# Kernel tuning notes

Hardware: AMD Instinct MI355X
Metric: run time of the kernel (lower is better)

## Reference

```python
import jax, jax.numpy as jnp
import numpy as np

C = 256
NUM_HEADS = 8
HEAD_DIM = C // NUM_HEADS
EPS = 1e-5


def setup_inputs() -> dict:
    key = jax.random.key(0)
    ks = jax.random.split(key, 12)
    b, h, w = 8, 64, 64
    s = 1.0 / np.sqrt(C)
    return {
        "cortical": jax.random.normal(ks[0], (b, C, h, w), jnp.float32),
        "subcortical": jax.random.normal(ks[1], (b, C, h, w), jnp.float32),
        "ventricular": jax.random.normal(ks[2], (b, C, h, w), jnp.float32),
        "in_proj_w": jax.random.uniform(ks[3], (3 * C, C), jnp.float32, -s, s),
        "in_proj_b": jnp.zeros((3 * C,), jnp.float32),
        "out_proj_w": jax.random.uniform(ks[4], (C, C), jnp.float32, -s, s),
        "out_proj_b": jnp.zeros((C,), jnp.float32),
        "ln_gamma": jnp.ones((C,), jnp.float32),
        "ln_beta": jnp.zeros((C,), jnp.float32),
        "conv_w": jax.random.uniform(ks[5], (C, 3 * C), jnp.float32, -1.0 / np.sqrt(3 * C), 1.0 / np.sqrt(3 * C)),
        "conv_b": jnp.zeros((C,), jnp.float32),
    }


def _forward(cortical, subcortical, ventricular,
             in_proj_w, in_proj_b, out_proj_w, out_proj_b,
             ln_gamma, ln_beta, conv_w, conv_b):
    b, c, h, w = cortical.shape
    # stack regions -> tokens of seq_len 3: (b,h,w,3,c) -> (N,3,c)
    regions = jnp.stack([cortical, subcortical, ventricular], axis=1)  # (b,3,c,h,w)
    x = regions.transpose(0, 3, 4, 1, 2).reshape(b * h * w, 3, c)
    # fused QKV projection
    qkv = x @ in_proj_w.T + in_proj_b  # (N,3,3c)
    q, k, v = jnp.split(qkv, 3, axis=-1)
    # split heads: (N,3,H,D)
    def heads(t):
        return t.reshape(-1, 3, NUM_HEADS, HEAD_DIM)
    q, k, v = heads(q), heads(k), heads(v)
    scores = jnp.einsum("nshd,nthd->nhst", q, k) / np.sqrt(HEAD_DIM)
    attn = jax.nn.softmax(scores, axis=-1)
    o = jnp.einsum("nhst,nthd->nshd", attn, v).reshape(-1, 3, c)
    o = o @ out_proj_w.T + out_proj_b
    # residual + LayerNorm over channels
    y = o + x
    mu = y.mean(-1, keepdims=True)
    var = y.var(-1, keepdims=True)
    y = (y - mu) * jax.lax.rsqrt(var + EPS) * ln_gamma + ln_beta
    # (N,3,c) -> (b,h,w,3c) region-major == torch cat along channel dim
    fused = y.reshape(b, h, w, 3 * c)
    out = fused @ conv_w.T + conv_b  # 1x1 conv as matmul
    return out.transpose(0, 3, 1, 2)  # (b,c,h,w)


def reference(cortical, subcortical, ventricular, in_proj_w, in_proj_b,
              out_proj_w, out_proj_b, ln_gamma, ln_beta, conv_w, conv_b):
    return _forward(cortical, subcortical, ventricular, in_proj_w, in_proj_b,
                    out_proj_w, out_proj_b, ln_gamma, ln_beta, conv_w, conv_b)
```

## Files before the change

### kernel.cpp

```cpp
#include <hip/hip_runtime.h>

typedef __bf16 bf16x8 __attribute__((ext_vector_type(8)));
typedef float  f32x4  __attribute__((ext_vector_type(4)));

#define XOFF 0
#define OOFF 49152
#define OBUFSZ 7680
#define PSOFF 64512
#define PQOFF 66048
#define MUOFF 67584
#define RSOFF 67968
#define SMEM_BYTES 68352

static __device__ __forceinline__ unsigned short f2b(float f) {
  __bf16 h = (__bf16)f;
  return __builtin_bit_cast(unsigned short, h);
}

__global__ void convert_weights(const float* __restrict__ w_in,
                                const float* __restrict__ w_out,
                                const float* __restrict__ w_conv,
                                __bf16* __restrict__ ws) {
  int gid = blockIdx.x * 256 + threadIdx.x;
  int i4 = gid * 4;
  const float* src;
  int off;
  if (i4 < 196608)      { src = w_in;   off = i4; }
  else if (i4 < 262144) { src = w_out;  off = i4 - 196608; }
  else                  { src = w_conv; off = i4 - 262144; }
  float4 f = *(const float4*)(src + off);
  ws[i4 + 0] = (__bf16)f.x;
  ws[i4 + 1] = (__bf16)f.y;
  ws[i4 + 2] = (__bf16)f.z;
  ws[i4 + 3] = (__bf16)f.w;
}

__global__ __launch_bounds__(256, 2) void crf_fused(
    const float* __restrict__ cort,
    const float* __restrict__ subc,
    const float* __restrict__ vent,
    const __bf16* __restrict__ w_in,
    const float* __restrict__ b_in,
    const __bf16* __restrict__ w_out,
    const float* __restrict__ b_out,
    const float* __restrict__ gamma,
    const float* __restrict__ beta,
    const __bf16* __restrict__ w_conv,
    const float* __restrict__ b_conv,
    float* __restrict__ out) {
  extern __shared__ char smem[];
  const int tid  = threadIdx.x;
  const int lane = tid & 63;
  const int wv   = tid >> 6;
  const int l15  = lane & 15;
  const int l4   = lane >> 4;
  const int blk  = blockIdx.x;
  const int img  = blk >> 7;
  const int pixbase = (blk & 127) << 5;
  const size_t base = (size_t)img * (256 * 4096) + pixbase;

  {
    const float* rp0 = cort + base;
    const float* rp1 = subc + base;
    const float* rp2 = vent + base;
#pragma unroll
    for (int si = 0; si < 3; ++si) {
      const float* rp = (si == 0) ? rp0 : (si == 1) ? rp1 : rp2;
#pragma unroll
      for (int t = 0; t < 16; ++t) {
        int idx = t * 256 + tid;
        int p   = idx & 31;
        int c   = (idx >> 5) * 2;
        float f0 = rp[(size_t)c * 4096 + p];
        float f1 = rp[(size_t)(c + 1) * 4096 + p];
        int m = si * 32 + p;
        unsigned off = ((unsigned)(m * 512 + c * 2)) ^ ((unsigned)(m & 7) << 4);
        unsigned pack = (unsigned)f2b(f0) | ((unsigned)f2b(f1) << 16);
        *(unsigned*)(smem + XOFF + off) = pack;
      }
    }
  }

  f32x4 accY[6][4] = {};

  __syncthreads();

  const int ph = wv & 1;
  const int hg = wv >> 1;
  const float SC = 0.17677669529663687f;

  for (int hh = 0; hh < 4; ++hh) {
    const int h = hg * 4 + hh;
    f32x4 acc[3][6] = {};
#pragma unroll
    for (int ks = 0; ks < 8; ++ks) {
      const int k0 = ks * 32;
      bf16x8 af[3], bfr[6];
#pragma unroll
      for (int s = 0; s < 3; ++s) {
        int m = s * 32 + ph * 16 + l15;
        unsigned off = ((unsigned)(m * 512 + (k0 + l4 * 8) * 2)) ^ ((unsigned)(m & 7) << 4);
        af[s] = *(const bf16x8*)(smem + XOFF + off);
      }
#pragma unroll
      for (int j = 0; j < 6; ++j) {
        int jb = (j >> 1) * 256 + h * 32 + (j & 1) * 16 + l15;
        bfr[j] = *(const bf16x8*)(w_in + (size_t)jb * 256 + k0 + l4 * 8);
      }
#pragma unroll
      for (int s = 0; s < 3; ++s)
#pragma unroll
        for (int j = 0; j < 6; ++j)
          acc[s][j] = __builtin_amdgcn_mfma_f32_16x16x32_bf16(af[s], bfr[j], acc[s][j], 0, 0, 0);
    }
#pragma unroll
    for (int jq = 0; jq < 2; ++jq) {
      float bq = b_in[h * 32 + jq * 16 + l15];
      float bk = b_in[256 + h * 32 + jq * 16 + l15];
      float bv = b_in[512 + h * 32 + jq * 16 + l15];
#pragma unroll
      for (int s = 0; s < 3; ++s)
#pragma unroll
        for (int r = 0; r < 4; ++r) {
          acc[s][jq][r]     += bq;
          acc[s][2 + jq][r] += bk;
          acc[s][4 + jq][r] += bv;
        }
    }
    char* ob = smem + OOFF + hg * OBUFSZ;
#pragma unroll
    for (int si = 0; si < 3; ++si) {
      float pp[3][4];
#pragma unroll
      for (int ti = 0; ti < 3; ++ti)
#pragma unroll
        for (int r = 0; r < 4; ++r)
          pp[ti][r] = acc[si][0][r] * acc[ti][2][r] + acc[si][1][r] * acc[ti][3][r];
#pragma unroll
      for (int mask = 1; mask <= 8; mask <<= 1)
#pragma unroll
        for (int ti = 0; ti < 3; ++ti)
#pragma unroll
          for (int r = 0; r < 4; ++r)
            pp[ti][r] += __shfl_xor(pp[ti][r], mask);
#pragma unroll
      for (int r = 0; r < 4; ++r) {
        float s0 = pp[0][r] * SC, s1 = pp[1][r] * SC, s2 = pp[2][r] * SC;
        float mx = fmaxf(fmaxf(s0, s1), s2);
        float e0 = __expf(s0 - mx), e1 = __expf(s1 - mx), e2 = __expf(s2 - mx);
        float inv = 1.f / (e0 + e1 + e2);
        e0 *= inv; e1 *= inv; e2 *= inv;
        int m = si * 32 + ph * 16 + l4 * 4 + r;
#pragma unroll
        for (int jq = 0; jq < 2; ++jq) {
          float ov = e0 * acc[0][4 + jq][r] + e1 * acc[1][4 + jq][r] + e2 * acc[2][4 + jq][r];
          *(__bf16*)(ob + m * 80 + (jq * 16 + l15) * 2) = (__bf16)ov;
        }
      }
    }
    __syncthreads();

#pragma unroll
    for (int g = 0; g < 2; ++g) {
      const char* obr = smem + OOFF + g * OBUFSZ;
      const int hB = g * 4 + hh;
      bf16x8 af2[6], bf2[4];
#pragma unroll
      for (int i = 0; i < 6; ++i)
        af2[i] = *(const bf16x8*)(obr + (i * 16 + l15) * 80 + l4 * 16);
#pragma unroll
      for (int j = 0; j < 4; ++j) {
        int jr = wv * 64 + j * 16 + l15;
        bf2[j] = *(const bf16x8*)(w_out + (size_t)jr * 256 + hB * 32 + l4 * 8);
      }
#pragma unroll
      for (int i = 0; i < 6; ++i)
#pragma unroll
        for (int j = 0; j < 4; ++j)
          accY[i][j] = __builtin_amdgcn_mfma_f32_16x16x32_bf16(af2[i], bf2[j], accY[i][j], 0, 0, 0);
    }
    __syncthreads();
  }

  float bo[4], gg[4], bb[4];
#pragma unroll
  for (int j = 0; j < 4; ++j) {
    int jc = wv * 64 + j * 16 + l15;
    bo[j] = b_out[jc];
    gg[j] = gamma[jc];
    bb[j] = beta[jc];
  }
#pragma unroll
  for (int i = 0; i < 6; ++i)
#pragma unroll
    for (int r = 0; r < 4; ++r) {
      int m = i * 16 + l4 * 4 + r;
      float s1 = 0.f, s2 = 0.f;
#pragma unroll
      for (int j = 0; j < 4; ++j) {
        int jc = wv * 64 + j * 16 + l15;
        unsigned xo = ((unsigned)(m * 512 + jc * 2)) ^ ((unsigned)(m & 7) << 4);
        float xv = (float)(*(const __bf16*)(smem + XOFF + xo));
        float v = accY[i][j][r] + bo[j] + xv;
        accY[i][j][r] = v;
        s1 += v;
        s2 += v * v;
      }
      s1 += __shfl_xor(s1, 1); s2 += __shfl_xor(s2, 1);
      s1 += __shfl_xor(s1, 2); s2 += __shfl_xor(s2, 2);
      s1 += __shfl_xor(s1, 4); s2 += __shfl_xor(s2, 4);
      s1 += __shfl_xor(s1, 8); s2 += __shfl_xor(s2, 8);
      if (l15 == 0) {
        *(float*)(smem + PSOFF + (m * 4 + wv) * 4) = s1;
        *(float*)(smem + PQOFF + (m * 4 + wv) * 4) = s2;
      }
    }
  __syncthreads();
  if (tid < 96) {
    float s = 0.f, q = 0.f;
#pragma unroll
    for (int j = 0; j < 4; ++j) {
      s += *(const float*)(smem + PSOFF + (tid * 4 + j) * 4);
      q += *(const float*)(smem + PQOFF + (tid * 4 + j) * 4);
    }
    float mu  = s * (1.f / 256.f);
    float var = q * (1.f / 256.f) - mu * mu;
    *(float*)(smem + MUOFF + tid * 4) = mu;
    *(float*)(smem + RSOFF + tid * 4) = rsqrtf(var + 1e-5f);
  }
  __syncthreads();
#pragma unroll
  for (int i = 0; i < 6; ++i)
#pragma unroll
    for (int r = 0; r < 4; ++r) {
      int m = i * 16 + l4 * 4 + r;
      float mu = *(const float*)(smem + MUOFF + m * 4);
      float rs = *(const float*)(smem + RSOFF + m * 4);
      int s = m >> 5, p = m & 31;
#pragma unroll
      for (int j = 0; j < 4; ++j) {
        int jc = wv * 64 + j * 16 + l15;
        float yv = (accY[i][j][r] - mu) * rs * gg[j] + bb[j];
        int kk = s * 256 + jc;
        unsigned off = ((unsigned)(p * 1536 + kk * 2)) ^ ((unsigned)(p & 7) << 4);
        *(__bf16*)(smem + XOFF + off) = (__bf16)yv;
      }
    }
  __syncthreads();

  {
    f32x4 accC[4][2] = {};
#pragma unroll 4
    for (int ks = 0; ks < 24; ++ks) {
      const int k0 = ks * 32;
      bf16x8 af[4], bfr2[2];
#pragma unroll
      for (int i = 0; i < 4; ++i) {
        int co = wv * 64 + i * 16 + l15;
        af[i] = *(const bf16x8*)(w_conv + (size_t)co * 768 + k0 + l4 * 8);
      }
#pragma unroll
      for (int j = 0; j < 2; ++j) {
        int p = j * 16 + l15;
        unsigned off = ((unsigned)(p * 1536 + (k0 + l4 * 8) * 2)) ^ ((unsigned)(p & 7) << 4);
        bfr2[j] = *(const bf16x8*)(smem + XOFF + off);
      }
#pragma unroll
      for (int i = 0; i < 4; ++i)
#pragma unroll
        for (int j = 0; j < 2; ++j)
          accC[i][j] = __builtin_amdgcn_mfma_f32_16x16x32_bf16(af[i], bfr2[j], accC[i][j], 0, 0, 0);
    }
#pragma unroll
    for (int i = 0; i < 4; ++i)
#pragma unroll
      for (int r = 0; r < 4; ++r) {
        int co = wv * 64 + i * 16 + l4 * 4 + r;
        float cb = b_conv[co];
#pragma unroll
        for (int j = 0; j < 2; ++j)
          out[((size_t)img * 256 + co) * 4096 + pixbase + j * 16 + l15] = accC[i][j][r] + cb;
      }
  }
}

extern "C" void kernel_launch(void* const* d_in, const int* in_sizes, int n_in,
                              void* d_out, int out_size, void* d_ws, size_t ws_size,
                              hipStream_t stream) {
  (void)in_sizes; (void)n_in; (void)out_size; (void)ws_size;
  const float* cort    = (const float*)d_in[0];
  const float* subc    = (const float*)d_in[1];
  const float* vent    = (const float*)d_in[2];
  const float* w_in_f  = (const float*)d_in[3];
  const float* b_in    = (const float*)d_in[4];
  const float* w_out_f = (const float*)d_in[5];
  const float* b_out   = (const float*)d_in[6];
  const float* gamma   = (const float*)d_in[7];
  const float* beta    = (const float*)d_in[8];
  const float* w_conv_f= (const float*)d_in[9];
  const float* b_conv  = (const float*)d_in[10];

  __bf16* ws = (__bf16*)d_ws;
  convert_weights<<<448, 256, 0, stream>>>(w_in_f, w_out_f, w_conv_f, ws);
  crf_fused<<<1024, 256, SMEM_BYTES, stream>>>(
      cort, subc, vent,
      ws,            b_in,
      ws + 196608,   b_out,
      gamma,         beta,
      ws + 262144,   b_conv,
      (float*)d_out);
}
```

Measured before the change: 204.4 us.

## Double-buffer attention output, prefetch QKV weights, vectorize input loads

The attention-output buffer is double-buffered per head iteration, which drops the second barrier per head loop, and its layout switches from padded rows to an XOR swizzle. QKV weight fragments are software-prefetched one k-step ahead into a register double buffer. The input-staging loop now reads float4 along pixels instead of scalar pairs. The bias adds are hoisted to the start of the head loop. The costs are more LDS (larger SMEM_BYTES), higher register pressure from the prefetch buffers, and scalar bf16 LDS stores during staging.

```diff
diff --git a/kernel.cpp b/kernel.cpp
--- a/kernel.cpp
+++ b/kernel.cpp
@@ -5,17 +5,13 @@
 
 #define XOFF 0
 #define OOFF 49152
-#define OBUFSZ 7680
-#define PSOFF 64512
-#define PQOFF 66048
-#define MUOFF 67584
-#define RSOFF 67968
-#define SMEM_BYTES 68352
-
-static __device__ __forceinline__ unsigned short f2b(float f) {
-  __bf16 h = (__bf16)f;
-  return __builtin_bit_cast(unsigned short, h);
-}
+#define OBSZ 6144
+#define PSOFF 73728
+#define PQOFF 75264
+#define MUOFF 76800
+#define RSOFF 77184
+#define SMEM_BYTES 77568
+#define OB(g,b) (smem + OOFF + ((g) * 2 + (b)) * OBSZ)
 
 __global__ void convert_weights(const float* __restrict__ w_in,
                                 const float* __restrict__ w_out,
@@ -67,16 +63,18 @@
     for (int si = 0; si < 3; ++si) {
       const float* rp = (si == 0) ? rp0 : (si == 1) ? rp1 : rp2;
 #pragma unroll
-      for (int t = 0; t < 16; ++t) {
+      for (int t = 0; t < 8; ++t) {
         int idx = t * 256 + tid;
-        int p   = idx & 31;
-        int c   = (idx >> 5) * 2;
-        float f0 = rp[(size_t)c * 4096 + p];
-        float f1 = rp[(size_t)(c + 1) * 4096 + p];
-        int m = si * 32 + p;
-        unsigned off = ((unsigned)(m * 512 + c * 2)) ^ ((unsigned)(m & 7) << 4);
-        unsigned pack = (unsigned)f2b(f0) | ((unsigned)f2b(f1) << 16);
-        *(unsigned*)(smem + XOFF + off) = pack;
+        int p4  = (idx & 7) * 4;
+        int c   = idx >> 3;
+        float4 f = *(const float4*)(rp + (size_t)c * 4096 + p4);
+#pragma unroll
+        for (int k = 0; k < 4; ++k) {
+          int m = si * 32 + p4 + k;
+          unsigned off = ((unsigned)(m * 512 + c * 2)) ^ ((unsigned)(m & 7) << 4);
+          float fv = (k == 0) ? f.x : (k == 1) ? f.y : (k == 2) ? f.z : f.w;
+          *(__bf16*)(smem + XOFF + off) = (__bf16)fv;
+        }
       }
     }
   }
@@ -91,11 +89,28 @@
 
   for (int hh = 0; hh < 4; ++hh) {
     const int h = hg * 4 + hh;
+    float bq0 = b_in[h * 32 + l15],       bq1 = b_in[h * 32 + 16 + l15];
+    float bk0 = b_in[256 + h * 32 + l15], bk1 = b_in[256 + h * 32 + 16 + l15];
+    float bv0 = b_in[512 + h * 32 + l15], bv1 = b_in[512 + h * 32 + 16 + l15];
+
     f32x4 acc[3][6] = {};
+    bf16x8 bb[2][6];
+#pragma unroll
+    for (int j = 0; j < 6; ++j) {
+      int jb = (j >> 1) * 256 + h * 32 + (j & 1) * 16 + l15;
+      bb[0][j] = *(const bf16x8*)(w_in + (size_t)jb * 256 + l4 * 8);
+    }
 #pragma unroll
     for (int ks = 0; ks < 8; ++ks) {
       const int k0 = ks * 32;
-      bf16x8 af[3], bfr[6];
+      if (ks < 7) {
+#pragma unroll
+        for (int j = 0; j < 6; ++j) {
+          int jb = (j >> 1) * 256 + h * 32 + (j & 1) * 16 + l15;
+          bb[(ks + 1) & 1][j] = *(const bf16x8*)(w_in + (size_t)jb * 256 + k0 + 32 + l4 * 8);
+        }
+      }
+      bf16x8 af[3];
 #pragma unroll
       for (int s = 0; s < 3; ++s) {
         int m = s * 32 + ph * 16 + l15;
@@ -103,31 +118,21 @@
         af[s] = *(const bf16x8*)(smem + XOFF + off);
       }
 #pragma unroll
-      for (int j = 0; j < 6; ++j) {
-        int jb = (j >> 1) * 256 + h * 32 + (j & 1) * 16 + l15;
-        bfr[j] = *(const bf16x8*)(w_in + (size_t)jb * 256 + k0 + l4 * 8);
-      }
-#pragma unroll
       for (int s = 0; s < 3; ++s)
 #pragma unroll
         for (int j = 0; j < 6; ++j)
-          acc[s][j] = __builtin_amdgcn_mfma_f32_16x16x32_bf16(af[s], bfr[j], acc[s][j], 0, 0, 0);
-    }
-#pragma unroll
-    for (int jq = 0; jq < 2; ++jq) {
-      float bq = b_in[h * 32 + jq * 16 + l15];
-      float bk = b_in[256 + h * 32 + jq * 16 + l15];
-      float bv = b_in[512 + h * 32 + jq * 16 + l15];
-#pragma unroll
-      for (int s = 0; s < 3; ++s)
-#pragma unroll
-        for (int r = 0; r < 4; ++r) {
-          acc[s][jq][r]     += bq;
-          acc[s][2 + jq][r] += bk;
-          acc[s][4 + jq][r] += bv;
-        }
-    }
-    char* ob = smem + OOFF + hg * OBUFSZ;
+          acc[s][j] = __builtin_amdgcn_mfma_f32_16x16x32_bf16(af[s], bb[ks & 1][j], acc[s][j], 0, 0, 0);
+    }
+#pragma unroll
+    for (int s = 0; s < 3; ++s)
+#pragma unroll
+      for (int r = 0; r < 4; ++r) {
+        acc[s][0][r] += bq0; acc[s][1][r] += bq1;
+        acc[s][2][r] += bk0; acc[s][3][r] += bk1;
+        acc[s][4][r] += bv0; acc[s][5][r] += bv1;
+      }
+
+    char* ob = OB(hg, hh & 1);
 #pragma unroll
     for (int si = 0; si < 3; ++si) {
       float pp[3][4];
@@ -154,41 +159,46 @@
 #pragma unroll
         for (int jq = 0; jq < 2; ++jq) {
           float ov = e0 * acc[0][4 + jq][r] + e1 * acc[1][4 + jq][r] + e2 * acc[2][4 + jq][r];
-          *(__bf16*)(ob + m * 80 + (jq * 16 + l15) * 2) = (__bf16)ov;
+          unsigned off = ((unsigned)(m * 64 + (jq * 16 + l15) * 2)) ^ ((unsigned)(m & 7) << 4);
+          *(__bf16*)(ob + off) = (__bf16)ov;
         }
       }
     }
     __syncthreads();
 
-#pragma unroll
-    for (int g = 0; g < 2; ++g) {
-      const char* obr = smem + OOFF + g * OBUFSZ;
-      const int hB = g * 4 + hh;
-      bf16x8 af2[6], bf2[4];
-#pragma unroll
-      for (int i = 0; i < 6; ++i)
-        af2[i] = *(const bf16x8*)(obr + (i * 16 + l15) * 80 + l4 * 16);
+    {
+      const int b = hh & 1;
+      bf16x8 afA[6], afB[6], bfA[4], bfB[4];
+#pragma unroll
+      for (int i = 0; i < 6; ++i) {
+        int row = i * 16 + l15;
+        unsigned off = ((unsigned)(row * 64 + l4 * 16)) ^ ((unsigned)(row & 7) << 4);
+        afA[i] = *(const bf16x8*)(OB(0, b) + off);
+        afB[i] = *(const bf16x8*)(OB(1, b) + off);
+      }
 #pragma unroll
       for (int j = 0; j < 4; ++j) {
         int jr = wv * 64 + j * 16 + l15;
-        bf2[j] = *(const bf16x8*)(w_out + (size_t)jr * 256 + hB * 32 + l4 * 8);
+        bfA[j] = *(const bf16x8*)(w_out + (size_t)jr * 256 + hh * 32 + l4 * 8);
+        bfB[j] = *(const bf16x8*)(w_out + (size_t)jr * 256 + (4 + hh) * 32 + l4 * 8);
       }
 #pragma unroll
       for (int i = 0; i < 6; ++i)
 #pragma unroll
-        for (int j = 0; j < 4; ++j)
-          accY[i][j] = __builtin_amdgcn_mfma_f32_16x16x32_bf16(af2[i], bf2[j], accY[i][j], 0, 0, 0);
-    }
-    __syncthreads();
-  }
-
-  float bo[4], gg[4], bb[4];
+        for (int j = 0; j < 4; ++j) {
+          accY[i][j] = __builtin_amdgcn_mfma_f32_16x16x32_bf16(afA[i], bfA[j], accY[i][j], 0, 0, 0);
+          accY[i][j] = __builtin_amdgcn_mfma_f32_16x16x32_bf16(afB[i], bfB[j], accY[i][j], 0, 0, 0);
+        }
+    }
+  }
+
+  float bo[4], gg[4], bb2[4];
 #pragma unroll
   for (int j = 0; j < 4; ++j) {
     int jc = wv * 64 + j * 16 + l15;
     bo[j] = b_out[jc];
     gg[j] = gamma[jc];
-    bb[j] = beta[jc];
+    bb2[j] = beta[jc];
   }
 #pragma unroll
   for (int i = 0; i < 6; ++i)
@@ -240,7 +250,7 @@
 #pragma unroll
       for (int j = 0; j < 4; ++j) {
         int jc = wv * 64 + j * 16 + l15;
-        float yv = (accY[i][j][r] - mu) * rs * gg[j] + bb[j];
+        float yv = (accY[i][j][r] - mu) * rs * gg[j] + bb2[j];
         int kk = s * 256 + jc;
         unsigned off = ((unsigned)(p * 1536 + kk * 2)) ^ ((unsigned)(p & 7) << 4);
         *(__bf16*)(smem + XOFF + off) = (__bf16)yv;
```

Result: slower. 240.1 us (+17.4%).

## Widen fused block to 1024 threads with one head per wave pair

Applied to the files above, without the earlier changes.

Each block now launches 16 waves instead of 4, so every head of the QKV and attention stage is handled at once by its own pair of waves instead of looping over heads. The per-head attention outputs are written into one full swizzled LDS tile, and out_proj is done as a single K=256 GEMM with each wave owning 16 output channels. The input load switches to float4 vector reads. This removes the per-head barrier loop and lowers register pressure per wave, but raises LDS use to about 109 KB per block, which limits residency to one block per CU.

```diff
diff --git a/kernel.cpp b/kernel.cpp
--- a/kernel.cpp
+++ b/kernel.cpp
@@ -5,12 +5,11 @@
 
 #define XOFF 0
 #define OOFF 49152
-#define OBUFSZ 7680
-#define PSOFF 64512
-#define PQOFF 66048
-#define MUOFF 67584
-#define RSOFF 67968
-#define SMEM_BYTES 68352
+#define PSOFF 98304
+#define PQOFF 104448
+#define MUOFF 110592
+#define RSOFF 110976
+#define SMEM_BYTES 111360
 
 static __device__ __forceinline__ unsigned short f2b(float f) {
   __bf16 h = (__bf16)f;
@@ -35,7 +34,7 @@
   ws[i4 + 3] = (__bf16)f.w;
 }
 
-__global__ __launch_bounds__(256, 2) void crf_fused(
+__global__ __launch_bounds__(1024) void crf_fused(
     const float* __restrict__ cort,
     const float* __restrict__ subc,
     const float* __restrict__ vent,
@@ -60,42 +59,35 @@
   const size_t base = (size_t)img * (256 * 4096) + pixbase;
 
   {
-    const float* rp0 = cort + base;
-    const float* rp1 = subc + base;
-    const float* rp2 = vent + base;
+    const int p4 = (tid & 7) * 4;
+    const int c  = (tid >> 3) * 2;
 #pragma unroll
     for (int si = 0; si < 3; ++si) {
-      const float* rp = (si == 0) ? rp0 : (si == 1) ? rp1 : rp2;
-#pragma unroll
-      for (int t = 0; t < 16; ++t) {
-        int idx = t * 256 + tid;
-        int p   = idx & 31;
-        int c   = (idx >> 5) * 2;
-        float f0 = rp[(size_t)c * 4096 + p];
-        float f1 = rp[(size_t)(c + 1) * 4096 + p];
-        int m = si * 32 + p;
+      const float* rp = (si == 0) ? cort : (si == 1) ? subc : vent;
+      rp += base;
+      float4 fa = *(const float4*)(rp + (size_t)c * 4096 + p4);
+      float4 fb = *(const float4*)(rp + (size_t)(c + 1) * 4096 + p4);
+#pragma unroll
+      for (int k = 0; k < 4; ++k) {
+        int m = si * 32 + p4 + k;
+        float va = (k == 0) ? fa.x : (k == 1) ? fa.y : (k == 2) ? fa.z : fa.w;
+        float vb = (k == 0) ? fb.x : (k == 1) ? fb.y : (k == 2) ? fb.z : fb.w;
         unsigned off = ((unsigned)(m * 512 + c * 2)) ^ ((unsigned)(m & 7) << 4);
-        unsigned pack = (unsigned)f2b(f0) | ((unsigned)f2b(f1) << 16);
-        *(unsigned*)(smem + XOFF + off) = pack;
-      }
-    }
-  }
-
-  f32x4 accY[6][4] = {};
-
-  __syncthreads();
-
-  const int ph = wv & 1;
-  const int hg = wv >> 1;
-  const float SC = 0.17677669529663687f;
-
-  for (int hh = 0; hh < 4; ++hh) {
-    const int h = hg * 4 + hh;
+        *(unsigned*)(smem + XOFF + off) = (unsigned)f2b(va) | ((unsigned)f2b(vb) << 16);
+      }
+    }
+  }
+  __syncthreads();
+
+  {
+    const int h  = wv >> 1;
+    const int ph = wv & 1;
+    const float SC = 0.17677669529663687f;
     f32x4 acc[3][6] = {};
 #pragma unroll
     for (int ks = 0; ks < 8; ++ks) {
       const int k0 = ks * 32;
-      bf16x8 af[3], bfr[6];
+      bf16x8 af[3];
 #pragma unroll
       for (int s = 0; s < 3; ++s) {
         int m = s * 32 + ph * 16 + l15;
@@ -105,13 +97,11 @@
 #pragma unroll
       for (int j = 0; j < 6; ++j) {
         int jb = (j >> 1) * 256 + h * 32 + (j & 1) * 16 + l15;
-        bfr[j] = *(const bf16x8*)(w_in + (size_t)jb * 256 + k0 + l4 * 8);
-      }
-#pragma unroll
-      for (int s = 0; s < 3; ++s)
-#pragma unroll
-        for (int j = 0; j < 6; ++j)
-          acc[s][j] = __builtin_amdgcn_mfma_f32_16x16x32_bf16(af[s], bfr[j], acc[s][j], 0, 0, 0);
+        bf16x8 bfr = *(const bf16x8*)(w_in + (size_t)jb * 256 + k0 + l4 * 8);
+#pragma unroll
+        for (int s = 0; s < 3; ++s)
+          acc[s][j] = __builtin_amdgcn_mfma_f32_16x16x32_bf16(af[s], bfr, acc[s][j], 0, 0, 0);
+      }
     }
 #pragma unroll
     for (int jq = 0; jq < 2; ++jq) {
@@ -127,7 +117,6 @@
           acc[s][4 + jq][r] += bv;
         }
     }
-    char* ob = smem + OOFF + hg * OBUFSZ;
 #pragma unroll
     for (int si = 0; si < 3; ++si) {
       float pp[3][4];
@@ -154,74 +143,59 @@
 #pragma unroll
         for (int jq = 0; jq < 2; ++jq) {
           float ov = e0 * acc[0][4 + jq][r] + e1 * acc[1][4 + jq][r] + e2 * acc[2][4 + jq][r];
-          *(__bf16*)(ob + m * 80 + (jq * 16 + l15) * 2) = (__bf16)ov;
+          int d = h * 32 + jq * 16 + l15;
+          unsigned off = ((unsigned)(m * 512 + d * 2)) ^ ((unsigned)(m & 7) << 4);
+          *(__bf16*)(smem + OOFF + off) = (__bf16)ov;
         }
       }
     }
-    __syncthreads();
-
-#pragma unroll
-    for (int g = 0; g < 2; ++g) {
-      const char* obr = smem + OOFF + g * OBUFSZ;
-      const int hB = g * 4 + hh;
-      bf16x8 af2[6], bf2[4];
-#pragma unroll
-      for (int i = 0; i < 6; ++i)
-        af2[i] = *(const bf16x8*)(obr + (i * 16 + l15) * 80 + l4 * 16);
-#pragma unroll
-      for (int j = 0; j < 4; ++j) {
-        int jr = wv * 64 + j * 16 + l15;
-        bf2[j] = *(const bf16x8*)(w_out + (size_t)jr * 256 + hB * 32 + l4 * 8);
-      }
-#pragma unroll
-      for (int i = 0; i < 6; ++i)
-#pragma unroll
-        for (int j = 0; j < 4; ++j)
-          accY[i][j] = __builtin_amdgcn_mfma_f32_16x16x32_bf16(af2[i], bf2[j], accY[i][j], 0, 0, 0);
-    }
-    __syncthreads();
-  }
-
-  float bo[4], gg[4], bb[4];
-#pragma unroll
-  for (int j = 0; j < 4; ++j) {
-    int jc = wv * 64 + j * 16 + l15;
-    bo[j] = b_out[jc];
-    gg[j] = gamma[jc];
-    bb[j] = beta[jc];
-  }
-#pragma unroll
-  for (int i = 0; i < 6; ++i)
-#pragma unroll
-    for (int r = 0; r < 4; ++r) {
-      int m = i * 16 + l4 * 4 + r;
-      float s1 = 0.f, s2 = 0.f;
-#pragma unroll
-      for (int j = 0; j < 4; ++j) {
-        int jc = wv * 64 + j * 16 + l15;
+  }
+  __syncthreads();
+
+  f32x4 accY[6] = {};
+#pragma unroll
+  for (int ks = 0; ks < 8; ++ks) {
+    const int k0 = ks * 32;
+    bf16x8 bfr = *(const bf16x8*)(w_out + (size_t)(wv * 16 + l15) * 256 + k0 + l4 * 8);
+#pragma unroll
+    for (int i = 0; i < 6; ++i) {
+      int m = i * 16 + l15;
+      unsigned off = ((unsigned)(m * 512 + (k0 + l4 * 8) * 2)) ^ ((unsigned)(m & 7) << 4);
+      bf16x8 af = *(const bf16x8*)(smem + OOFF + off);
+      accY[i] = __builtin_amdgcn_mfma_f32_16x16x32_bf16(af, bfr, accY[i], 0, 0, 0);
+    }
+  }
+
+  {
+    const int jc = wv * 16 + l15;
+    float bo = b_out[jc];
+#pragma unroll
+    for (int i = 0; i < 6; ++i)
+#pragma unroll
+      for (int r = 0; r < 4; ++r) {
+        int m = i * 16 + l4 * 4 + r;
         unsigned xo = ((unsigned)(m * 512 + jc * 2)) ^ ((unsigned)(m & 7) << 4);
         float xv = (float)(*(const __bf16*)(smem + XOFF + xo));
-        float v = accY[i][j][r] + bo[j] + xv;
-        accY[i][j][r] = v;
-        s1 += v;
-        s2 += v * v;
-      }
-      s1 += __shfl_xor(s1, 1); s2 += __shfl_xor(s2, 1);
-      s1 += __shfl_xor(s1, 2); s2 += __shfl_xor(s2, 2);
-      s1 += __shfl_xor(s1, 4); s2 += __shfl_xor(s2, 4);
-      s1 += __shfl_xor(s1, 8); s2 += __shfl_xor(s2, 8);
-      if (l15 == 0) {
-        *(float*)(smem + PSOFF + (m * 4 + wv) * 4) = s1;
-        *(float*)(smem + PQOFF + (m * 4 + wv) * 4) = s2;
-      }
-    }
+        float v = accY[i][r] + bo + xv;
+        accY[i][r] = v;
+        float s1 = v, s2 = v * v;
+        s1 += __shfl_xor(s1, 1); s2 += __shfl_xor(s2, 1);
+        s1 += __shfl_xor(s1, 2); s2 += __shfl_xor(s2, 2);
+        s1 += __shfl_xor(s1, 4); s2 += __shfl_xor(s2, 4);
+        s1 += __shfl_xor(s1, 8); s2 += __shfl_xor(s2, 8);
+        if (l15 == 0) {
+          *(float*)(smem + PSOFF + (m * 16 + wv) * 4) = s1;
+          *(float*)(smem + PQOFF + (m * 16 + wv) * 4) = s2;
+        }
+      }
+  }
   __syncthreads();
   if (tid < 96) {
     float s = 0.f, q = 0.f;
 #pragma unroll
-    for (int j = 0; j < 4; ++j) {
-      s += *(const float*)(smem + PSOFF + (tid * 4 + j) * 4);
-      q += *(const float*)(smem + PQOFF + (tid * 4 + j) * 4);
+    for (int j = 0; j < 16; ++j) {
+      s += *(const float*)(smem + PSOFF + (tid * 16 + j) * 4);
+      q += *(const float*)(smem + PQOFF + (tid * 16 + j) * 4);
     }
     float mu  = s * (1.f / 256.f);
     float var = q * (1.f / 256.f) - mu * mu;
@@ -229,58 +203,48 @@
     *(float*)(smem + RSOFF + tid * 4) = rsqrtf(var + 1e-5f);
   }
   __syncthreads();
-#pragma unroll
-  for (int i = 0; i < 6; ++i)
-#pragma unroll
-    for (int r = 0; r < 4; ++r) {
-      int m = i * 16 + l4 * 4 + r;
-      float mu = *(const float*)(smem + MUOFF + m * 4);
-      float rs = *(const float*)(smem + RSOFF + m * 4);
-      int s = m >> 5, p = m & 31;
-#pragma unroll
-      for (int j = 0; j < 4; ++j) {
-        int jc = wv * 64 + j * 16 + l15;
-        float yv = (accY[i][j][r] - mu) * rs * gg[j] + bb[j];
+  {
+    const int jc = wv * 16 + l15;
+    float gg = gamma[jc];
+    float bb = beta[jc];
+#pragma unroll
+    for (int i = 0; i < 6; ++i)
+#pragma unroll
+      for (int r = 0; r < 4; ++r) {
+        int m = i * 16 + l4 * 4 + r;
+        float mu = *(const float*)(smem + MUOFF + m * 4);
+        float rs = *(const float*)(smem + RSOFF + m * 4);
+        float yv = (accY[i][r] - mu) * rs * gg + bb;
+        int p = m & 31, s = m >> 5;
         int kk = s * 256 + jc;
         unsigned off = ((unsigned)(p * 1536 + kk * 2)) ^ ((unsigned)(p & 7) << 4);
         *(__bf16*)(smem + XOFF + off) = (__bf16)yv;
       }
-    }
-  __syncthreads();
-
-  {
-    f32x4 accC[4][2] = {};
+  }
+  __syncthreads();
+
+  {
+    f32x4 accC[2] = {};
 #pragma unroll 4
     for (int ks = 0; ks < 24; ++ks) {
       const int k0 = ks * 32;
-      bf16x8 af[4], bfr2[2];
-#pragma unroll
-      for (int i = 0; i < 4; ++i) {
-        int co = wv * 64 + i * 16 + l15;
-        af[i] = *(const bf16x8*)(w_conv + (size_t)co * 768 + k0 + l4 * 8);
-      }
+      bf16x8 af = *(const bf16x8*)(w_conv + (size_t)(wv * 16 + l15) * 768 + k0 + l4 * 8);
 #pragma unroll
       for (int j = 0; j < 2; ++j) {
         int p = j * 16 + l15;
         unsigned off = ((unsigned)(p * 1536 + (k0 + l4 * 8) * 2)) ^ ((unsigned)(p & 7) << 4);
-        bfr2[j] = *(const bf16x8*)(smem + XOFF + off);
-      }
-#pragma unroll
-      for (int i = 0; i < 4; ++i)
-#pragma unroll
-        for (int j = 0; j < 2; ++j)
-          accC[i][j] = __builtin_amdgcn_mfma_f32_16x16x32_bf16(af[i], bfr2[j], accC[i][j], 0, 0, 0);
-    }
-#pragma unroll
-    for (int i = 0; i < 4; ++i)
-#pragma unroll
-      for (int r = 0; r < 4; ++r) {
-        int co = wv * 64 + i * 16 + l4 * 4 + r;
-        float cb = b_conv[co];
-#pragma unroll
-        for (int j = 0; j < 2; ++j)
-          out[((size_t)img * 256 + co) * 4096 + pixbase + j * 16 + l15] = accC[i][j][r] + cb;
-      }
+        bf16x8 bfr = *(const bf16x8*)(smem + XOFF + off);
+        accC[j] = __builtin_amdgcn_mfma_f32_16x16x32_bf16(af, bfr, accC[j], 0, 0, 0);
+      }
+    }
+#pragma unroll
+    for (int r = 0; r < 4; ++r) {
+      int co = wv * 16 + l4 * 4 + r;
+      float cb = b_conv[co];
+#pragma unroll
+      for (int j = 0; j < 2; ++j)
+        out[((size_t)img * 256 + co) * 4096 + pixbase + j * 16 + l15] = accC[j][r] + cb;
+    }
   }
 }
 
@@ -302,7 +266,7 @@
 
   __bf16* ws = (__bf16*)d_ws;
   convert_weights<<<448, 256, 0, stream>>>(w_in_f, w_out_f, w_conv_f, ws);
-  crf_fused<<<1024, 256, SMEM_BYTES, stream>>>(
+  crf_fused<<<1024, 1024, SMEM_BYTES, stream>>>(
       cort, subc, vent,
       ws,            b_in,
       ws + 196608,   b_out,
```

New measurement: 249.4 us, median of 2. 1.22x slower.

## Split fused kernel into QKV-attention and projection-LN-conv kernels via global buffer

Applied to the files above, without the earlier changes.

Splits the single fused kernel into two. The first computes QKV and attention and writes the per-tile attention output to a workspace buffer in global memory. The second reloads that buffer, runs the out-projection, rereads the residual input in fp32 from the original tensors, then applies LayerNorm and the 1x1 conv. The aim is less shared memory and fewer registers per kernel so more blocks fit per CU (launch bounds raised to 3), and removing the per-head barriers between attention and the out-projection. The cost is an extra global round trip of about 48 MB, a second read of the inputs for the residual, and an extra launch.

```diff
diff --git a/kernel.cpp b/kernel.cpp
--- a/kernel.cpp
+++ b/kernel.cpp
@@ -3,14 +3,7 @@
 typedef __bf16 bf16x8 __attribute__((ext_vector_type(8)));
 typedef float  f32x4  __attribute__((ext_vector_type(4)));
 
-#define XOFF 0
-#define OOFF 49152
-#define OBUFSZ 7680
-#define PSOFF 64512
-#define PQOFF 66048
-#define MUOFF 67584
-#define RSOFF 67968
-#define SMEM_BYTES 68352
+#define OTILE 49152
 
 static __device__ __forceinline__ unsigned short f2b(float f) {
   __bf16 h = (__bf16)f;
@@ -35,20 +28,14 @@
   ws[i4 + 3] = (__bf16)f.w;
 }
 
-__global__ __launch_bounds__(256, 2) void crf_fused(
+__global__ __launch_bounds__(256, 3) void k1_qkv_attn(
     const float* __restrict__ cort,
     const float* __restrict__ subc,
     const float* __restrict__ vent,
     const __bf16* __restrict__ w_in,
     const float* __restrict__ b_in,
-    const __bf16* __restrict__ w_out,
-    const float* __restrict__ b_out,
-    const float* __restrict__ gamma,
-    const float* __restrict__ beta,
-    const __bf16* __restrict__ w_conv,
-    const float* __restrict__ b_conv,
-    float* __restrict__ out) {
-  extern __shared__ char smem[];
+    char* __restrict__ o_ws) {
+  __shared__ char smem[49152];
   const int tid  = threadIdx.x;
   const int lane = tid & 63;
   const int wv   = tid >> 6;
@@ -59,32 +46,25 @@
   const int pixbase = (blk & 127) << 5;
   const size_t base = (size_t)img * (256 * 4096) + pixbase;
 
-  {
-    const float* rp0 = cort + base;
-    const float* rp1 = subc + base;
-    const float* rp2 = vent + base;
-#pragma unroll
-    for (int si = 0; si < 3; ++si) {
-      const float* rp = (si == 0) ? rp0 : (si == 1) ? rp1 : rp2;
-#pragma unroll
-      for (int t = 0; t < 16; ++t) {
-        int idx = t * 256 + tid;
-        int p   = idx & 31;
-        int c   = (idx >> 5) * 2;
-        float f0 = rp[(size_t)c * 4096 + p];
-        float f1 = rp[(size_t)(c + 1) * 4096 + p];
-        int m = si * 32 + p;
-        unsigned off = ((unsigned)(m * 512 + c * 2)) ^ ((unsigned)(m & 7) << 4);
-        unsigned pack = (unsigned)f2b(f0) | ((unsigned)f2b(f1) << 16);
-        *(unsigned*)(smem + XOFF + off) = pack;
-      }
-    }
-  }
-
-  f32x4 accY[6][4] = {};
-
-  __syncthreads();
-
+#pragma unroll
+  for (int si = 0; si < 3; ++si) {
+    const float* rp = (si == 0) ? cort : (si == 1) ? subc : vent;
+    rp += base;
+#pragma unroll
+    for (int t = 0; t < 16; ++t) {
+      int idx = t * 256 + tid;
+      int p   = idx & 31;
+      int c   = (idx >> 5) * 2;
+      float f0 = rp[(size_t)c * 4096 + p];
+      float f1 = rp[(size_t)(c + 1) * 4096 + p];
+      int m = si * 32 + p;
+      unsigned off = ((unsigned)(m * 512 + c * 2)) ^ ((unsigned)(m & 7) << 4);
+      *(unsigned*)(smem + off) = (unsigned)f2b(f0) | ((unsigned)f2b(f1) << 16);
+    }
+  }
+  __syncthreads();
+
+  char* otile = o_ws + (size_t)blk * OTILE;
   const int ph = wv & 1;
   const int hg = wv >> 1;
   const float SC = 0.17677669529663687f;
@@ -95,23 +75,21 @@
 #pragma unroll
     for (int ks = 0; ks < 8; ++ks) {
       const int k0 = ks * 32;
-      bf16x8 af[3], bfr[6];
+      bf16x8 af[3];
 #pragma unroll
       for (int s = 0; s < 3; ++s) {
         int m = s * 32 + ph * 16 + l15;
         unsigned off = ((unsigned)(m * 512 + (k0 + l4 * 8) * 2)) ^ ((unsigned)(m & 7) << 4);
-        af[s] = *(const bf16x8*)(smem + XOFF + off);
+        af[s] = *(const bf16x8*)(smem + off);
       }
 #pragma unroll
       for (int j = 0; j < 6; ++j) {
         int jb = (j >> 1) * 256 + h * 32 + (j & 1) * 16 + l15;
-        bfr[j] = *(const bf16x8*)(w_in + (size_t)jb * 256 + k0 + l4 * 8);
-      }
-#pragma unroll
-      for (int s = 0; s < 3; ++s)
-#pragma unroll
-        for (int j = 0; j < 6; ++j)
-          acc[s][j] = __builtin_amdgcn_mfma_f32_16x16x32_bf16(af[s], bfr[j], acc[s][j], 0, 0, 0);
+        bf16x8 bfr = *(const bf16x8*)(w_in + (size_t)jb * 256 + k0 + l4 * 8);
+#pragma unroll
+        for (int s = 0; s < 3; ++s)
+          acc[s][j] = __builtin_amdgcn_mfma_f32_16x16x32_bf16(af[s], bfr, acc[s][j], 0, 0, 0);
+      }
     }
 #pragma unroll
     for (int jq = 0; jq < 2; ++jq) {
@@ -127,7 +105,6 @@
           acc[s][4 + jq][r] += bv;
         }
     }
-    char* ob = smem + OOFF + hg * OBUFSZ;
 #pragma unroll
     for (int si = 0; si < 3; ++si) {
       float pp[3][4];
@@ -154,32 +131,74 @@
 #pragma unroll
         for (int jq = 0; jq < 2; ++jq) {
           float ov = e0 * acc[0][4 + jq][r] + e1 * acc[1][4 + jq][r] + e2 * acc[2][4 + jq][r];
-          *(__bf16*)(ob + m * 80 + (jq * 16 + l15) * 2) = (__bf16)ov;
+          int d = h * 32 + jq * 16 + l15;
+          unsigned off = ((unsigned)(m * 512 + d * 2)) ^ ((unsigned)(m & 7) << 4);
+          *(__bf16*)(otile + off) = (__bf16)ov;
         }
       }
     }
-    __syncthreads();
-
-#pragma unroll
-    for (int g = 0; g < 2; ++g) {
-      const char* obr = smem + OOFF + g * OBUFSZ;
-      const int hB = g * 4 + hh;
-      bf16x8 af2[6], bf2[4];
-#pragma unroll
-      for (int i = 0; i < 6; ++i)
-        af2[i] = *(const bf16x8*)(obr + (i * 16 + l15) * 80 + l4 * 16);
-#pragma unroll
-      for (int j = 0; j < 4; ++j) {
-        int jr = wv * 64 + j * 16 + l15;
-        bf2[j] = *(const bf16x8*)(w_out + (size_t)jr * 256 + hB * 32 + l4 * 8);
-      }
-#pragma unroll
-      for (int i = 0; i < 6; ++i)
-#pragma unroll
-        for (int j = 0; j < 4; ++j)
-          accY[i][j] = __builtin_amdgcn_mfma_f32_16x16x32_bf16(af2[i], bf2[j], accY[i][j], 0, 0, 0);
-    }
-    __syncthreads();
+  }
+}
+
+#define PSOFF 49152
+#define PQOFF 50688
+#define MUOFF 52224
+#define RSOFF 52608
+
+__global__ __launch_bounds__(256, 3) void k2_proj_ln_conv(
+    const float* __restrict__ cort,
+    const float* __restrict__ subc,
+    const float* __restrict__ vent,
+    const char* __restrict__ o_ws,
+    const __bf16* __restrict__ w_out,
+    const float* __restrict__ b_out,
+    const float* __restrict__ gamma,
+    const float* __restrict__ beta,
+    const __bf16* __restrict__ w_conv,
+    const float* __restrict__ b_conv,
+    float* __restrict__ out) {
+  __shared__ char smem[52992];
+  const int tid  = threadIdx.x;
+  const int lane = tid & 63;
+  const int wv   = tid >> 6;
+  const int l15  = lane & 15;
+  const int l4   = lane >> 4;
+  const int blk  = blockIdx.x;
+  const int img  = blk >> 7;
+  const int pixbase = (blk & 127) << 5;
+  const size_t base = (size_t)img * (256 * 4096) + pixbase;
+
+  {
+    const char* src = o_ws + (size_t)blk * OTILE;
+#pragma unroll
+    for (int t = 0; t < 12; ++t) {
+      int off = t * 4096 + tid * 16;
+      *(bf16x8*)(smem + off) = *(const bf16x8*)(src + off);
+    }
+  }
+  __syncthreads();
+
+  f32x4 accY[6][4] = {};
+#pragma unroll
+  for (int ks = 0; ks < 8; ++ks) {
+    const int k0 = ks * 32;
+    bf16x8 af[6], bfr[4];
+#pragma unroll
+    for (int i = 0; i < 6; ++i) {
+      int m = i * 16 + l15;
+      unsigned off = ((unsigned)(m * 512 + (k0 + l4 * 8) * 2)) ^ ((unsigned)(m & 7) << 4);
+      af[i] = *(const bf16x8*)(smem + off);
+    }
+#pragma unroll
+    for (int j = 0; j < 4; ++j) {
+      int jr = wv * 64 + j * 16 + l15;
+      bfr[j] = *(const bf16x8*)(w_out + (size_t)jr * 256 + k0 + l4 * 8);
+    }
+#pragma unroll
+    for (int i = 0; i < 6; ++i)
+#pragma unroll
+      for (int j = 0; j < 4; ++j)
+        accY[i][j] = __builtin_amdgcn_mfma_f32_16x16x32_bf16(af[i], bfr[j], accY[i][j], 0, 0, 0);
   }
 
   float bo[4], gg[4], bb[4];
@@ -191,16 +210,17 @@
     bb[j] = beta[jc];
   }
 #pragma unroll
-  for (int i = 0; i < 6; ++i)
+  for (int i = 0; i < 6; ++i) {
+    const float* rp = ((i >> 1) == 0) ? cort : ((i >> 1) == 1) ? subc : vent;
 #pragma unroll
     for (int r = 0; r < 4; ++r) {
       int m = i * 16 + l4 * 4 + r;
+      int p = m & 31;
       float s1 = 0.f, s2 = 0.f;
 #pragma unroll
       for (int j = 0; j < 4; ++j) {
         int jc = wv * 64 + j * 16 + l15;
-        unsigned xo = ((unsigned)(m * 512 + jc * 2)) ^ ((unsigned)(m & 7) << 4);
-        float xv = (float)(*(const __bf16*)(smem + XOFF + xo));
+        float xv = rp[base + (size_t)jc * 4096 + p];
         float v = accY[i][j][r] + bo[j] + xv;
         accY[i][j][r] = v;
         s1 += v;
@@ -215,6 +235,7 @@
         *(float*)(smem + PQOFF + (m * 4 + wv) * 4) = s2;
       }
     }
+  }
   __syncthreads();
   if (tid < 96) {
     float s = 0.f, q = 0.f;
@@ -243,7 +264,7 @@
         float yv = (accY[i][j][r] - mu) * rs * gg[j] + bb[j];
         int kk = s * 256 + jc;
         unsigned off = ((unsigned)(p * 1536 + kk * 2)) ^ ((unsigned)(p & 7) << 4);
-        *(__bf16*)(smem + XOFF + off) = (__bf16)yv;
+        *(__bf16*)(smem + off) = (__bf16)yv;
       }
     }
   __syncthreads();
@@ -263,7 +284,7 @@
       for (int j = 0; j < 2; ++j) {
         int p = j * 16 + l15;
         unsigned off = ((unsigned)(p * 1536 + (k0 + l4 * 8) * 2)) ^ ((unsigned)(p & 7) << 4);
-        bfr2[j] = *(const bf16x8*)(smem + XOFF + off);
+        bfr2[j] = *(const bf16x8*)(smem + off);
       }
 #pragma unroll
       for (int i = 0; i < 4; ++i)
@@ -300,13 +321,12 @@
   const float* w_conv_f= (const float*)d_in[9];
   const float* b_conv  = (const float*)d_in[10];
 
-  __bf16* ws = (__bf16*)d_ws;
-  convert_weights<<<448, 256, 0, stream>>>(w_in_f, w_out_f, w_conv_f, ws);
-  crf_fused<<<1024, 256, SMEM_BYTES, stream>>>(
-      cort, subc, vent,
-      ws,            b_in,
-      ws + 196608,   b_out,
-      gamma,         beta,
-      ws + 262144,   b_conv,
-      (float*)d_out);
-}
+  __bf16* wsb = (__bf16*)d_ws;
+  char*   o_ws = (char*)d_ws + (1 << 20);
+
+  convert_weights<<<448, 256, 0, stream>>>(w_in_f, w_out_f, w_conv_f, wsb);
+  k1_qkv_attn<<<1024, 256, 0, stream>>>(cort, subc, vent, wsb, b_in, o_ws);
+  k2_proj_ln_conv<<<1024, 256, 0, stream>>>(cort, subc, vent, o_ws,
+                                            wsb + 196608, b_out, gamma, beta,
+                                            wsb + 262144, b_conv, (float*)d_out);
+}
```

Result: slower. 355.4 us (+73.8%).
